# Kernel tuning notes

Measured on AMD Instinct MI355X. Metric: run time of the kernel, lower is better.

Reference implementation:

```python
import jax, jax.numpy as jnp
import numpy as np

B, T, I, H, O = 4096, 512, 15, 64, 1


def setup_inputs() -> dict:
    key = jax.random.key(0)
    ks = jax.random.split(key, 7)
    s_rnn = 1.0 / np.sqrt(H)  # torch nn.RNN init scale
    s_fc = 1.0 / np.sqrt(H)   # torch nn.Linear init scale (fan_in = H)
    u = lambda k, shape, s: jax.random.uniform(k, shape, jnp.float32, -s, s)
    return {
        "x": jax.random.normal(ks[0], (B, T, I), jnp.float32),
        "W_ih": u(ks[1], (H, I), s_rnn),
        "W_hh": u(ks[2], (H, H), s_rnn),
        "b_ih": u(ks[3], (H,), s_rnn),
        "b_hh": u(ks[4], (H,), s_rnn),
        "fc_w": u(ks[5], (O, H), s_fc),
        "fc_b": u(ks[6], (O,), s_fc),
    }


def reference(x, W_ih, W_hh, b_ih, b_hh, fc_w, fc_b):
    # Precompute input projection for all timesteps in one GEMM: [B, T, H]
    xp = jnp.einsum("bti,hi->bth", x, W_ih) + b_ih + b_hh

    def step(h, xt):  # h: [B, H], xt: [B, H]
        h_new = jnp.tanh(xt + h @ W_hh.T)
        return h_new, None

    h0 = jnp.zeros((x.shape[0], W_hh.shape[0]), x.dtype)
    hT, _ = jax.lax.scan(step, h0, jnp.swapaxes(xp, 0, 1))  # scan over time
    # last-step linear head: [B, O]
    return hT @ fc_w.T + fc_b
```

## Files before the change

kernel.cpp:

```cpp
#include <hip/hip_runtime.h>


#define T_STEPS 512
#define I_DIM 15
#define BPW 16
#define WIN 64
#define NWIN (T_STEPS / WIN)

typedef _Float16 half8 __attribute__((ext_vector_type(8)));
typedef __attribute__((ext_vector_type(4))) float float4v;
typedef __attribute__((ext_vector_type(4))) unsigned int uint4v;

union H8U { half8 h; uint4v u; };

__device__ __forceinline__ unsigned pkh(float a, float b) {
    union { _Float16 h; unsigned short u; } A, B;
    A.h = (_Float16)a;
    B.h = (_Float16)b;
    return (unsigned)A.u | ((unsigned)B.u << 16);
}
__device__ __forceinline__ unsigned pkz(float a, float b) {
    auto r = __builtin_amdgcn_cvt_pkrtz(a, b);
    unsigned u;
    __builtin_memcpy(&u, &r, 4);
    return u;
}

#define EPI_PAIR(BK, JA, JB, HH) do {                                             \
    _Pragma("unroll")                                                             \
    for (int r = 0; r < 4; r++) {                                                 \
        float ex = __builtin_amdgcn_exp2f(Aa[BK][JA][r]);                         \
        hfin[JA][r] = __builtin_fmaf(-2.f, __builtin_amdgcn_rcpf(ex + 1.f), 1.f); \
    }                                                                             \
    _Pragma("unroll")                                                             \
    for (int r = 0; r < 4; r++) {                                                 \
        float ex = __builtin_amdgcn_exp2f(Aa[BK][JB][r]);                         \
        hfin[JB][r] = __builtin_fmaf(-2.f, __builtin_amdgcn_rcpf(ex + 1.f), 1.f); \
    }                                                                             \
    HH.u[0] = pkz(hfin[JA][0], hfin[JA][1]);                                      \
    HH.u[1] = pkz(hfin[JA][2], hfin[JA][3]);                                      \
    HH.u[2] = pkz(hfin[JB][0], hfin[JB][1]);                                      \
    HH.u[3] = pkz(hfin[JB][2], hfin[JB][3]);                                      \
} while (0)

#define STEP(X, Y, XF) do {                                                       \
    Aa[X][0] = __builtin_amdgcn_mfma_f32_16x16x32_f16(whf[0][2], XF, cbv[0], 0, 0, 0); \
    Aa[X][1] = __builtin_amdgcn_mfma_f32_16x16x32_f16(whf[1][2], XF, cbv[1], 0, 0, 0); \
    Aa[X][2] = __builtin_amdgcn_mfma_f32_16x16x32_f16(whf[2][2], XF, cbv[2], 0, 0, 0); \
    Aa[X][3] = __builtin_amdgcn_mfma_f32_16x16x32_f16(whf[3][2], XF, cbv[3], 0, 0, 0); \
    EPI_PAIR(Y, 2, 3, hh1);                                                       \
    _Pragma("unroll")                                                             \
    for (int jt = 0; jt < 4; jt++)                                                \
        Aa[X][jt] = __builtin_amdgcn_mfma_f32_16x16x32_f16(whf[jt][0], hh0.h, Aa[X][jt], 0, 0, 0); \
    _Pragma("unroll")                                                             \
    for (int jt = 0; jt < 4; jt++)                                                \
        Aa[X][jt] = __builtin_amdgcn_mfma_f32_16x16x32_f16(whf[jt][1], hh1.h, Aa[X][jt], 0, 0, 0); \
    EPI_PAIR(X, 0, 1, hh0);                                                       \
} while (0)

#define FILL(w) do {                                                              \
    const int ptid = tid - 64;                                                    \
    _Pragma("unroll 1")                                                           \
    for (int idx = ptid; idx < 16 * WIN; idx += 192) {                            \
        const int t  = idx & (WIN - 1);                                           \
        const int nn = idx >> 6;                                                  \
        const float* row = x + ((size_t)(b0 + nn) * T_STEPS + ((w) * WIN + t)) * I_DIM; \
        float v[16];                                                              \
        __builtin_memcpy(v, row, 60);                                             \
        v[15] = 0.f;                                                              \
        xls[(w) & 1][t][nn] = (uint4v){ pkh(v[0], v[1]),  pkh(v[2], v[3]),        \
                                        pkh(v[4], v[5]),  pkh(v[6], v[7]) };      \
        xls[(w) & 1][t][nn + 16] = (uint4v){ pkh(v[8], v[9]),   pkh(v[10], v[11]),\
                                             pkh(v[12], v[13]), pkh(v[14], v[15]) }; \
    }                                                                             \
} while (0)

#define CONSUME(w) do {                                                           \
    const uint4v* Wb = &xls[(w) & 1][0][lane & 31];                               \
    uint4v xc = Wb[0];                                                            \
    _Pragma("unroll 1")                                                           \
    for (int tt = 0; tt < WIN; tt += 2) {                                         \
        uint4v xp1 = Wb[(tt + 1) * 32];                   \
        H8U xA; xA.u = xc;                                                        \
        STEP(0, 1, xA.h);                                                         \
        int i2 = (tt + 2 < WIN) ? tt + 2 : WIN - 1;                               \
        xc = Wb[i2 * 32];                                 \
        H8U xB; xB.u = xp1;                                                       \
        STEP(1, 0, xB.h);                                                         \
    }                                                                             \
} while (0)

__global__ __launch_bounds__(256, 1) void rnn_fused(
    const float* __restrict__ x,
    const float* __restrict__ W_ih,
    const float* __restrict__ W_hh,
    const float* __restrict__ b_ih,
    const float* __restrict__ b_hh,
    const float* __restrict__ fc_w,
    const float* __restrict__ fc_b,
    float* __restrict__ out)
{
    __shared__ uint4v xls[2][WIN][32];

    const int tid  = threadIdx.x;
    const int wave = tid >> 6;
    const int lane = tid & 63;
    const int q = lane >> 4;
    const int n = lane & 15;
    const int b0 = blockIdx.x * BPW;
    const float K = 2.8853900817779268f;

    half8 whf[4][3];
    float4v cbv[4];
    #pragma unroll
    for (int jt = 0; jt < 4; jt++) {
        const int jcol = 32*(jt>>1) + 8*(n>>2) + 4*(jt&1) + (n&3);
        #pragma unroll
        for (int c = 0; c < 3; c++) {
            #pragma unroll
            for (int e = 0; e < 8; e++) {
                const int k = c*32 + q*8 + e;
                float w = 0.f;
                if (k < 64)      w = W_hh[jcol*64 + k] * K;
                else if (k < 79) w = W_ih[jcol*15 + (k - 64)] * K;
                whf[jt][c][e] = (_Float16)w;
            }
        }
        #pragma unroll
        for (int r = 0; r < 4; r++) {
            const int jr = 32*(jt>>1) + 8*q + 4*(jt&1) + r;
            cbv[jt][r] = K * (b_ih[jr] + b_hh[jr]);
        }
    }

    H8U hh0, hh1;
    hh0.u = (uint4v){0,0,0,0};
    hh1.u = (uint4v){0,0,0,0};
    float4v Aa[2][4];
    #pragma unroll
    for (int jt = 0; jt < 4; jt++) {
        Aa[0][jt] = (float4v){0.f,0.f,0.f,0.f};
        Aa[1][jt] = (float4v){0.f,0.f,0.f,0.f};
    }
    float hfin[4][4];

    if (wave != 0) FILL(0);
    __syncthreads();
    #pragma unroll 1
    for (int k = 1; k < NWIN; k++) {
        if (wave != 0) FILL(k);
        else           CONSUME(k - 1);
        __syncthreads();
    }
    if (wave == 0) {
        CONSUME(NWIN - 1);
        EPI_PAIR(1, 2, 3, hh1);

        float s = 0.f;
        #pragma unroll
        for (int jt = 0; jt < 4; jt++) {
            #pragma unroll
            for (int r = 0; r < 4; r++) {
                const int jr = 32*(jt>>1) + 8*q + 4*(jt&1) + r;
                s = __builtin_fmaf(hfin[jt][r], fc_w[jr], s);
            }
        }
        s += __shfl_xor(s, 16, 64);
        s += __shfl_xor(s, 32, 64);
        if (q == 0) out[b0 + n] = s + fc_b[0];
    }
}

extern "C" void kernel_launch(void* const* d_in, const int* in_sizes, int n_in,
                              void* d_out, int out_size, void* d_ws, size_t ws_size,
                              hipStream_t stream) {
    const float* x    = (const float*)d_in[0];
    const float* W_ih = (const float*)d_in[1];
    const float* W_hh = (const float*)d_in[2];
    const float* b_ih = (const float*)d_in[3];
    const float* b_hh = (const float*)d_in[4];
    const float* fc_w = (const float*)d_in[5];
    const float* fc_b = (const float*)d_in[6];
    float* out = (float*)d_out;

    rnn_fused<<<4096 / BPW, 256, 0, stream>>>(x, W_ih, W_hh, b_ih, b_hh,
                                              fc_w, fc_b, out);
}
```

Measured before the change: 307.8 us.

## Split hidden-state tiles across four waves with LDS exchange and per-step barriers

Each of the four waves now owns one 16-column tile of the hidden state and computes its three MFMAs per timestep, instead of a single wave doing all twelve while the others only load x. Hidden state is exchanged through a double-buffered LDS array with a block barrier every step. Input rows stream through a small LDS ring that waves refill in rotation, with register prefetch several steps ahead. This shortens the per-step serial chain but adds 512 barriers and LDS round-trips on the recurrence critical path.

```diff
diff --git a/kernel.cpp b/kernel.cpp
--- a/kernel.cpp
+++ b/kernel.cpp
@@ -4,8 +4,7 @@
 #define T_STEPS 512
 #define I_DIM 15
 #define BPW 16
-#define WIN 64
-#define NWIN (T_STEPS / WIN)
+#define RING 16
 
 typedef _Float16 half8 __attribute__((ext_vector_type(8)));
 typedef __attribute__((ext_vector_type(4))) float float4v;
@@ -26,70 +25,6 @@
     return u;
 }
 
-#define EPI_PAIR(BK, JA, JB, HH) do {                                             \
-    _Pragma("unroll")                                                             \
-    for (int r = 0; r < 4; r++) {                                                 \
-        float ex = __builtin_amdgcn_exp2f(Aa[BK][JA][r]);                         \
-        hfin[JA][r] = __builtin_fmaf(-2.f, __builtin_amdgcn_rcpf(ex + 1.f), 1.f); \
-    }                                                                             \
-    _Pragma("unroll")                                                             \
-    for (int r = 0; r < 4; r++) {                                                 \
-        float ex = __builtin_amdgcn_exp2f(Aa[BK][JB][r]);                         \
-        hfin[JB][r] = __builtin_fmaf(-2.f, __builtin_amdgcn_rcpf(ex + 1.f), 1.f); \
-    }                                                                             \
-    HH.u[0] = pkz(hfin[JA][0], hfin[JA][1]);                                      \
-    HH.u[1] = pkz(hfin[JA][2], hfin[JA][3]);                                      \
-    HH.u[2] = pkz(hfin[JB][0], hfin[JB][1]);                                      \
-    HH.u[3] = pkz(hfin[JB][2], hfin[JB][3]);                                      \
-} while (0)
-
-#define STEP(X, Y, XF) do {                                                       \
-    Aa[X][0] = __builtin_amdgcn_mfma_f32_16x16x32_f16(whf[0][2], XF, cbv[0], 0, 0, 0); \
-    Aa[X][1] = __builtin_amdgcn_mfma_f32_16x16x32_f16(whf[1][2], XF, cbv[1], 0, 0, 0); \
-    Aa[X][2] = __builtin_amdgcn_mfma_f32_16x16x32_f16(whf[2][2], XF, cbv[2], 0, 0, 0); \
-    Aa[X][3] = __builtin_amdgcn_mfma_f32_16x16x32_f16(whf[3][2], XF, cbv[3], 0, 0, 0); \
-    EPI_PAIR(Y, 2, 3, hh1);                                                       \
-    _Pragma("unroll")                                                             \
-    for (int jt = 0; jt < 4; jt++)                                                \
-        Aa[X][jt] = __builtin_amdgcn_mfma_f32_16x16x32_f16(whf[jt][0], hh0.h, Aa[X][jt], 0, 0, 0); \
-    _Pragma("unroll")                                                             \
-    for (int jt = 0; jt < 4; jt++)                                                \
-        Aa[X][jt] = __builtin_amdgcn_mfma_f32_16x16x32_f16(whf[jt][1], hh1.h, Aa[X][jt], 0, 0, 0); \
-    EPI_PAIR(X, 0, 1, hh0);                                                       \
-} while (0)
-
-#define FILL(w) do {                                                              \
-    const int ptid = tid - 64;                                                    \
-    _Pragma("unroll 1")                                                           \
-    for (int idx = ptid; idx < 16 * WIN; idx += 192) {                            \
-        const int t  = idx & (WIN - 1);                                           \
-        const int nn = idx >> 6;                                                  \
-        const float* row = x + ((size_t)(b0 + nn) * T_STEPS + ((w) * WIN + t)) * I_DIM; \
-        float v[16];                                                              \
-        __builtin_memcpy(v, row, 60);                                             \
-        v[15] = 0.f;                                                              \
-        xls[(w) & 1][t][nn] = (uint4v){ pkh(v[0], v[1]),  pkh(v[2], v[3]),        \
-                                        pkh(v[4], v[5]),  pkh(v[6], v[7]) };      \
-        xls[(w) & 1][t][nn + 16] = (uint4v){ pkh(v[8], v[9]),   pkh(v[10], v[11]),\
-                                             pkh(v[12], v[13]), pkh(v[14], v[15]) }; \
-    }                                                                             \
-} while (0)
-
-#define CONSUME(w) do {                                                           \
-    const uint4v* Wb = &xls[(w) & 1][0][lane & 31];                               \
-    uint4v xc = Wb[0];                                                            \
-    _Pragma("unroll 1")                                                           \
-    for (int tt = 0; tt < WIN; tt += 2) {                                         \
-        uint4v xp1 = Wb[(tt + 1) * 32];                   \
-        H8U xA; xA.u = xc;                                                        \
-        STEP(0, 1, xA.h);                                                         \
-        int i2 = (tt + 2 < WIN) ? tt + 2 : WIN - 1;                               \
-        xc = Wb[i2 * 32];                                 \
-        H8U xB; xB.u = xp1;                                                       \
-        STEP(1, 0, xB.h);                                                         \
-    }                                                                             \
-} while (0)
-
 __global__ __launch_bounds__(256, 1) void rnn_fused(
     const float* __restrict__ x,
     const float* __restrict__ W_ih,
@@ -100,7 +35,9 @@
     const float* __restrict__ fc_b,
     float* __restrict__ out)
 {
-    __shared__ uint4v xls[2][WIN][32];
+    __shared__ uint4v xring[RING][32];
+    __shared__ uint2  hx[2][4][64];
+    __shared__ float  psum[4][16];
 
     const int tid  = threadIdx.x;
     const int wave = tid >> 6;
@@ -108,67 +45,110 @@
     const int q = lane >> 4;
     const int n = lane & 15;
     const int b0 = blockIdx.x * BPW;
+    const int jt = wave;
     const float K = 2.8853900817779268f;
 
-    half8 whf[4][3];
-    float4v cbv[4];
+    half8 whf[3];
+    float4v cbv;
+    float fcwv[4];
+    const int jcol = 32*(jt>>1) + 8*(n>>2) + 4*(jt&1) + (n&3);
     #pragma unroll
-    for (int jt = 0; jt < 4; jt++) {
-        const int jcol = 32*(jt>>1) + 8*(n>>2) + 4*(jt&1) + (n&3);
+    for (int c = 0; c < 3; c++) {
         #pragma unroll
-        for (int c = 0; c < 3; c++) {
+        for (int e = 0; e < 8; e++) {
+            const int k = c*32 + q*8 + e;
+            float w = 0.f;
+            if (k < 64)      w = W_hh[jcol*64 + k] * K;
+            else if (k < 79) w = W_ih[jcol*15 + (k - 64)] * K;
+            whf[c][e] = (_Float16)w;
+        }
+    }
+    #pragma unroll
+    for (int r = 0; r < 4; r++) {
+        const int jr = 32*(jt>>1) + 8*q + 4*(jt&1) + r;
+        cbv[r]  = K * (b_ih[jr] + b_hh[jr]);
+        fcwv[r] = fc_w[jr];
+    }
+
+    const float* xrow = x + (size_t)(b0 + n) * (T_STEPS * I_DIM);
+
+    if (lane < 16) {
+        #pragma unroll
+        for (int j = 0; j < 2; j++) {
+            const int s = wave + 4*j;
+            float v[16];
+            __builtin_memcpy(v, xrow + (size_t)s * I_DIM, 60);
+            v[15] = 0.f;
+            xring[s & (RING-1)][n] = (uint4v){ pkh(v[0],v[1]), pkh(v[2],v[3]),
+                                               pkh(v[4],v[5]), pkh(v[6],v[7]) };
+            xring[s & (RING-1)][n + 16] = (uint4v){ pkh(v[8],v[9]),  pkh(v[10],v[11]),
+                                                    pkh(v[12],v[13]), pkh(v[14],v[15]) };
+        }
+    }
+    hx[1][wave][lane] = uint2{0u, 0u};
+    float rowbuf[15];
+    if (lane < 16)
+        __builtin_memcpy(rowbuf, xrow + (size_t)(wave + 8) * I_DIM, 60);
+
+    asm volatile("s_waitcnt lgkmcnt(0)\n\ts_barrier" ::: "memory");
+
+    uint4v xf = xring[0][lane & 31];
+    float4v acc;
+    float hfin[4];
+
+    for (int it = 0; it < T_STEPS / 4; ++it) {
+        #pragma unroll
+        for (int u = 0; u < 4; ++u) {
+            const int t = it * 4 + u;
+            const uint2 h0a = hx[(t+1)&1][0][lane];
+            const uint2 h0b = hx[(t+1)&1][1][lane];
+            const uint2 h1a = hx[(t+1)&1][2][lane];
+            const uint2 h1b = hx[(t+1)&1][3][lane];
+            const uint4v xfn = xring[(t+1)&(RING-1)][lane & 31];
+
+            H8U xb_; xb_.u = xf;
+            acc = __builtin_amdgcn_mfma_f32_16x16x32_f16(whf[2], xb_.h, cbv, 0, 0, 0);
+
+            if (wave == u) {
+                if (lane < 16) {
+                    const int s = t + 8;
+                    xring[s & (RING-1)][n] = (uint4v){ pkh(rowbuf[0],rowbuf[1]), pkh(rowbuf[2],rowbuf[3]),
+                                                       pkh(rowbuf[4],rowbuf[5]), pkh(rowbuf[6],rowbuf[7]) };
+                    xring[s & (RING-1)][n + 16] = (uint4v){ pkh(rowbuf[8],rowbuf[9]),   pkh(rowbuf[10],rowbuf[11]),
+                                                            pkh(rowbuf[12],rowbuf[13]), pkh(rowbuf[14], 0.f) };
+                    int tl = t + 12; if (tl > T_STEPS - 1) tl = T_STEPS - 1;
+                    __builtin_memcpy(rowbuf, xrow + (size_t)tl * I_DIM, 60);
+                }
+            }
+
+            H8U hh0; hh0.u = (uint4v){h0a.x, h0a.y, h0b.x, h0b.y};
+            acc = __builtin_amdgcn_mfma_f32_16x16x32_f16(whf[0], hh0.h, acc, 0, 0, 0);
+            H8U hh1; hh1.u = (uint4v){h1a.x, h1a.y, h1b.x, h1b.y};
+            acc = __builtin_amdgcn_mfma_f32_16x16x32_f16(whf[1], hh1.h, acc, 0, 0, 0);
+
             #pragma unroll
-            for (int e = 0; e < 8; e++) {
-                const int k = c*32 + q*8 + e;
-                float w = 0.f;
-                if (k < 64)      w = W_hh[jcol*64 + k] * K;
-                else if (k < 79) w = W_ih[jcol*15 + (k - 64)] * K;
-                whf[jt][c][e] = (_Float16)w;
+            for (int r = 0; r < 4; r++) {
+                float ex = __builtin_amdgcn_exp2f(acc[r]);
+                hfin[r] = __builtin_fmaf(-2.f, __builtin_amdgcn_rcpf(ex + 1.f), 1.f);
             }
-        }
-        #pragma unroll
-        for (int r = 0; r < 4; r++) {
-            const int jr = 32*(jt>>1) + 8*q + 4*(jt&1) + r;
-            cbv[jt][r] = K * (b_ih[jr] + b_hh[jr]);
+            uint2 hp; hp.x = pkz(hfin[0], hfin[1]); hp.y = pkz(hfin[2], hfin[3]);
+            hx[t&1][wave][lane] = hp;
+
+            asm volatile("s_waitcnt lgkmcnt(0)\n\ts_barrier" ::: "memory");
+            xf = xfn;
         }
     }
 
-    H8U hh0, hh1;
-    hh0.u = (uint4v){0,0,0,0};
-    hh1.u = (uint4v){0,0,0,0};
-    float4v Aa[2][4];
+    float s = 0.f;
     #pragma unroll
-    for (int jt = 0; jt < 4; jt++) {
-        Aa[0][jt] = (float4v){0.f,0.f,0.f,0.f};
-        Aa[1][jt] = (float4v){0.f,0.f,0.f,0.f};
-    }
-    float hfin[4][4];
-
-    if (wave != 0) FILL(0);
+    for (int r = 0; r < 4; r++) s = __builtin_fmaf(hfin[r], fcwv[r], s);
+    s += __shfl_xor(s, 16, 64);
+    s += __shfl_xor(s, 32, 64);
+    if (lane < 16) psum[wave][n] = s;
     __syncthreads();
-    #pragma unroll 1
-    for (int k = 1; k < NWIN; k++) {
-        if (wave != 0) FILL(k);
-        else           CONSUME(k - 1);
-        __syncthreads();
-    }
-    if (wave == 0) {
-        CONSUME(NWIN - 1);
-        EPI_PAIR(1, 2, 3, hh1);
-
-        float s = 0.f;
-        #pragma unroll
-        for (int jt = 0; jt < 4; jt++) {
-            #pragma unroll
-            for (int r = 0; r < 4; r++) {
-                const int jr = 32*(jt>>1) + 8*q + 4*(jt&1) + r;
-                s = __builtin_fmaf(hfin[jt][r], fc_w[jr], s);
-            }
-        }
-        s += __shfl_xor(s, 16, 64);
-        s += __shfl_xor(s, 32, 64);
-        if (q == 0) out[b0 + n] = s + fc_b[0];
-    }
+    if (tid < 16)
+        out[b0 + tid] = psum[0][tid] + psum[1][tid] + psum[2][tid]
+                      + psum[3][tid] + fc_b[0];
 }
 
 extern "C" void kernel_launch(void* const* d_in, const int* in_sizes, int n_in,
```

After: 272.5 us. 11.5% less time.
